# Kernel tuning notes

Hardware: AMD Instinct MI355X
Metric: run time of the kernel (lower is better)

Reference implementation:

```python
import jax, jax.numpy as jnp
import numpy as np

N_QUBITS = 256
N_LAYERS = 8
BATCH = 65536


def _ln(h, w, b):
    mu = jnp.mean(h, axis=-1, keepdims=True)
    var = jnp.mean((h - mu) ** 2, axis=-1, keepdims=True)
    return (h - mu) * jax.lax.rsqrt(var + 1e-5) * w + b


def setup_inputs() -> dict:
    key = jax.random.key(0)
    ks = jax.random.split(key, 22)
    Q = N_QUBITS
    s = 0.05
    f = jnp.float32
    return {
        "x": jax.random.normal(ks[0], (BATCH, Q), f),
        # type-0 sublayers (layers 0,3,6): Linear(Q,3Q)+LN+GELU+Linear(3Q,Q)
        "dense0_w1": jax.random.normal(ks[1], (3, Q, 3 * Q), f) * s,
        "dense0_b1": jnp.zeros((3, 3 * Q), f),
        "ln_w": jnp.ones((3, 3 * Q), f),
        "ln_b": jnp.zeros((3, 3 * Q), f),
        "dense0_w2": jax.random.normal(ks[2], (3, 3 * Q, Q), f) * s,
        "dense0_b2": jnp.zeros((3, Q), f),
        # type-1 sublayers (layers 1,4,7): Linear(Q,2Q)+SiLU+Linear(2Q,Q)
        "dense1_w1": jax.random.normal(ks[3], (3, Q, 2 * Q), f) * s,
        "dense1_b1": jnp.zeros((3, 2 * Q), f),
        "dense1_w2": jax.random.normal(ks[4], (3, 2 * Q, Q), f) * s,
        "dense1_b2": jnp.zeros((3, Q), f),
        # attention sublayers (layers 2,5): in_proj (qkv) + out_proj, heads=2, seq_len=1
        "attn_wqkv": jax.random.normal(ks[5], (2, Q, 3 * Q), f) * s,
        "attn_bqkv": jnp.zeros((2, 3 * Q), f),
        "attn_wo": jax.random.normal(ks[6], (2, Q, Q), f) * s,
        "attn_bo": jnp.zeros((2, Q), f),
        # per-layer gate params and entanglement matrices (torch randn init)
        "gate_params": jax.random.normal(ks[7], (N_LAYERS, Q, 6), f),
        "ent": jax.random.normal(ks[8], (N_LAYERS, Q, Q), f) * s,
        # nonlinear ops (4 = n_layers//2): Linear+Tanh+Linear
        "nl_w1": jax.random.normal(ks[9], (4, Q, Q), f) * s,
        "nl_b1": jnp.zeros((4, Q), f),
        "nl_w2": jax.random.normal(ks[10], (4, Q, Q), f) * s,
        "nl_b2": jnp.zeros((4, Q), f),
    }


def _forward(x, dense0_w1, dense0_b1, ln_w, ln_b, dense0_w2, dense0_b2,
             dense1_w1, dense1_b1, dense1_w2, dense1_b2,
             attn_wqkv, attn_bqkv, attn_wo, attn_bo,
             gate_params, ent, nl_w1, nl_b1, nl_w2, nl_b2):
    Q = N_QUBITS
    cur = x
    for li in range(N_LAYERS):
        res = cur
        t = li % 3
        if t == 0:
            i = li // 3
            h = cur @ dense0_w1[i] + dense0_b1[i]
            h = _ln(h, ln_w[i], ln_b[i])
            h = jax.nn.gelu(h, approximate=False)  # torch nn.GELU default (erf)
            cur = h @ dense0_w2[i] + dense0_b2[i]
        elif t == 1:
            i = (li - 1) // 3
            h = jax.nn.silu(cur @ dense1_w1[i] + dense1_b1[i])
            cur = h @ dense1_w2[i] + dense1_b2[i]
        else:
            i = (li - 2) // 3
            # seq_len == 1: softmax over a single key is identically 1, so
            # attended == v; q/k projections contribute zero (incl. gradient).
            qkv = cur @ attn_wqkv[i] + attn_bqkv[i]
            v = qkv[:, 2 * Q:]
            cur = v @ attn_wo[i] + attn_bo[i]
        # fused per-qubit gate effects (vectorized over qubits & batch)
        p = gate_params[li]  # [Q, 6]
        lin = jnp.sin(p[:, 0]) + jnp.cos(p[:, 1]) + jnp.tanh(p[:, 2])  # [Q]
        gate = (lin * cur
                + 0.5 * jnp.sin(p[:, 3] * cur + p[:, 4])
                + 0.5 * jnp.cos(p[:, 5] * cur)) / 4.0
        entangled = cur @ jnp.tanh(ent[li])
        cur = (cur + 0.3 * gate + 0.2 * entangled) / 1.5
        if li % 2 == 1:
            j = li // 2  # 0..3, always < 4 here
            nl = jnp.tanh(cur @ nl_w1[j] + nl_b1[j]) @ nl_w2[j] + nl_b2[j]
            cur = cur + 0.1 * nl
        alpha = 0.8 if li < N_LAYERS // 2 else 0.6
        cur = alpha * cur + (1.0 - alpha) * res
        cur = cur / (jnp.linalg.norm(cur, axis=1, keepdims=True) + 1e-8)
        cur = jnp.tanh(cur)
    return cur


def reference(x, dense0_w1, dense0_b1, ln_w, ln_b, dense0_w2, dense0_b2,
              dense1_w1, dense1_b1, dense1_w2, dense1_b2,
              attn_wqkv, attn_bqkv, attn_wo, attn_bo,
              gate_params, ent, nl_w1, nl_b1, nl_w2, nl_b2):
    return _forward(x, dense0_w1, dense0_b1, ln_w, ln_b, dense0_w2, dense0_b2,
                    dense1_w1, dense1_b1, dense1_w2, dense1_b2,
                    attn_wqkv, attn_bqkv, attn_wo, attn_bo,
                    gate_params, ent, nl_w1, nl_b1, nl_w2, nl_b2)
```

## Files before the change

kernel.cpp:

```cpp
#include <hip/hip_runtime.h>
#include <stdint.h>

#define DI __device__ __forceinline__

typedef __bf16 bf16;
typedef __bf16 bf16x8 __attribute__((ext_vector_type(8)));
typedef float  f32x4  __attribute__((ext_vector_type(4)));

constexpr int Q = 256;
constexpr int BATCH = 65536;
constexpr int TM = 64;
constexpr int THREADS = 256;
constexpr int NW = 4;
constexpr int MT = 4;
constexpr int NBLK = BATCH / TM;
constexpr int SC = Q + 8;

constexpr int W0A_OFF = 0;
constexpr int W0B_OFF = W0A_OFF + 3*768*256;
constexpr int W1A_OFF = W0B_OFF + 3*256*768;
constexpr int W1B_OFF = W1A_OFF + 3*512*256;
constexpr int WV_OFF  = W1B_OFF + 3*256*512;
constexpr int WO_OFF  = WV_OFF  + 2*65536;
constexpr int ATF_OFF = WO_OFF  + 2*65536;
constexpr int ENT_OFF = ATF_OFF + 2*65536;
constexpr int NL1_OFF = ENT_OFF + 8*65536;
constexpr int NL2_OFF = NL1_OFF + 4*65536;
constexpr int WEND    = NL2_OFF + 4*65536;
constexpr size_t F32_BYTE_OFF = (((size_t)WEND*2) + 255) & ~(size_t)255;

constexpr int P_D0B1 = 0;
constexpr int P_LNW  = P_D0B1 + 3*768;
constexpr int P_LNB  = P_LNW  + 3*768;
constexpr int P_D0B2 = P_LNB  + 3*768;
constexpr int P_D1B1 = P_D0B2 + 3*256;
constexpr int P_D1B2 = P_D1B1 + 3*512;
constexpr int P_BQV  = P_D1B2 + 3*256;
constexpr int P_BO   = P_BQV  + 2*256;
constexpr int P_NB1  = P_BO   + 2*256;
constexpr int P_NB2  = P_NB1  + 4*256;
constexpr int P_GLIN = P_NB2  + 4*256;
constexpr int P_GP3  = P_GLIN + 8*256;
constexpr int P_GP4  = P_GP3  + 8*256;
constexpr int P_GP5  = P_GP4  + 8*256;
constexpr int P_PACK_END = P_GP5 + 8*256;
constexpr int P_BAT  = P_PACK_END;
constexpr int P_TOT  = P_BAT + 2*256;
constexpr size_t FLAG_OFF = F32_BYTE_OFF + (size_t)P_TOT*4;

DI float ldf(const void* p, size_t idx, int f32) {
  return f32 ? ((const float*)p)[idx] : (float)((const bf16*)p)[idx];
}

DI float tanh_fast(float x) {
  float ax = fabsf(x);
  float e  = __expf(-2.0f * ax);
  float r  = (1.0f - e) / (1.0f + e);
  return copysignf(r, x);
}

DI float gelu_f(float x) {
  float ax = fabsf(x) * 0.70710678118654752f;
  float t  = 1.0f / (1.0f + 0.3275911f * ax);
  float y  = t*(0.254829592f + t*(-0.284496736f + t*(1.421413741f +
             t*(-1.453152027f + t*1.061405429f))));
  float er = copysignf(1.0f - y * __expf(-ax*ax), x);
  return 0.5f * x * (1.0f + er);
}

DI f32x4 mfma_bf16(uint4 a, uint4 b, f32x4 c) {
  return __builtin_amdgcn_mfma_f32_16x16x32_bf16(
      __builtin_bit_cast(bf16x8, a), __builtin_bit_cast(bf16x8, b), c, 0, 0, 0);
}

template<int NJ>
DI void zero_acc(f32x4 (&a)[MT][NJ]) {
#pragma unroll
  for (int i = 0; i < MT; ++i)
#pragma unroll
    for (int j = 0; j < NJ; ++j) a[i][j] = f32x4{0.f, 0.f, 0.f, 0.f};
}

template<int NJ>
DI void gemm_k256(const bf16* A, const bf16* __restrict__ Bt, int kdb, int koff,
                  f32x4 (&acc)[MT][NJ], int wave, int quad, int l16) {
  const bf16* ar[MT];
#pragma unroll
  for (int mt = 0; mt < MT; ++mt) ar[mt] = A + (mt*16 + l16)*SC + quad*8;
  const bf16* br[NJ];
#pragma unroll
  for (int nj = 0; nj < NJ; ++nj)
    br[nj] = Bt + (size_t)((nj*NW + wave)*16 + l16)*kdb + koff + quad*8;
#pragma unroll
  for (int ks = 0; ks < 8; ++ks) {
    uint4 av[MT];
#pragma unroll
    for (int mt = 0; mt < MT; ++mt) av[mt] = *(const uint4*)(ar[mt] + ks*32);
#pragma unroll
    for (int nj = 0; nj < NJ; ++nj) {
      uint4 bv = *(const uint4*)(br[nj] + ks*32);
#pragma unroll
      for (int mt = 0; mt < MT; ++mt) acc[mt][nj] = mfma_bf16(av[mt], bv, acc[mt][nj]);
    }
  }
}

template<int NJ>
DI void gemm_k256r(const bf16* A, const bf16* __restrict__ Bt, int kdb, int koff,
                   f32x4 (&acc)[MT][NJ], int wave, int quad, int l16) {
  const bf16* ar[MT];
#pragma unroll
  for (int mt = 0; mt < MT; ++mt) ar[mt] = A + (mt*16 + l16)*SC + quad*8;
  const bf16* br[NJ];
#pragma unroll
  for (int nj = 0; nj < NJ; ++nj)
    br[nj] = Bt + (size_t)((nj*NW + wave)*16 + l16)*kdb + koff + quad*8;
#pragma unroll
  for (int ks = 7; ks >= 0; --ks) {
    uint4 av[MT];
#pragma unroll
    for (int mt = 0; mt < MT; ++mt) av[mt] = *(const uint4*)(ar[mt] + ks*32);
#pragma unroll
    for (int nj = 0; nj < NJ; ++nj) {
      uint4 bv = *(const uint4*)(br[nj] + ks*32);
#pragma unroll
      for (int mt = 0; mt < MT; ++mt) acc[mt][nj] = mfma_bf16(av[mt], bv, acc[mt][nj]);
    }
  }
}

template<int NJ>
DI void addbias(f32x4 (&a)[MT][NJ], const float* __restrict__ b, int wave, int l16) {
#pragma unroll
  for (int nj = 0; nj < NJ; ++nj) {
    float bb = b[(nj*NW + wave)*16 + l16];
#pragma unroll
    for (int mt = 0; mt < MT; ++mt)
#pragma unroll
      for (int reg = 0; reg < 4; ++reg) a[mt][nj][reg] += bb;
  }
}

template<int NJ>
DI void store_t(bf16* dst, const f32x4 (&a)[MT][NJ], int wave, int quad, int l16) {
#pragma unroll
  for (int nj = 0; nj < NJ; ++nj) {
    int col = (nj*NW + wave)*16 + l16;
#pragma unroll
    for (int mt = 0; mt < MT; ++mt)
#pragma unroll
      for (int reg = 0; reg < 4; ++reg)
        dst[(mt*16 + quad*4 + reg)*SC + col] = (bf16)a[mt][nj][reg];
  }
}

__global__ void detect_dtype(const uint16_t* __restrict__ xr, int* __restrict__ flag) {
  __shared__ int s_max;
  if (threadIdx.x == 0) s_max = 0;
  __syncthreads();
  int e = 0;
  for (int i = threadIdx.x; i < 4096; i += 256) {
    int ex = (xr[2*i] >> 7) & 0xFF;
    e = e > ex ? e : ex;
  }
  atomicMax(&s_max, e);
  __syncthreads();
  if (threadIdx.x == 0) *flag = (s_max >= 140) ? 1 : 0;
}

__global__ void pack_weights(const void* __restrict__ d0w1, const void* __restrict__ d0w2,
                             const void* __restrict__ d1w1, const void* __restrict__ d1w2,
                             const void* __restrict__ wqkv, const void* __restrict__ wo,
                             const void* __restrict__ ent,  const void* __restrict__ nl1,
                             const void* __restrict__ nl2,  bf16* __restrict__ wsb,
                             const int* __restrict__ flag) {
  const int f32 = *flag;
  int job = blockIdx.y;
  const void* src; int mi, K, N, srcN, col0 = 0, dtanh = 0; long dst;
  if      (job < 3)  { src=d0w1; mi=job;    K=256; N=768; srcN=768; dst=W0A_OFF + (long)mi*768*256; }
  else if (job < 6)  { src=d0w2; mi=job-3;  K=768; N=256; srcN=256; dst=W0B_OFF + (long)mi*256*768; }
  else if (job < 9)  { src=d1w1; mi=job-6;  K=256; N=512; srcN=512; dst=W1A_OFF + (long)mi*512*256; }
  else if (job < 12) { src=d1w2; mi=job-9;  K=512; N=256; srcN=256; dst=W1B_OFF + (long)mi*256*512; }
  else if (job < 14) { src=wqkv; mi=job-12; K=256; N=256; srcN=768; col0=512; dst=WV_OFF + (long)mi*65536; }
  else if (job < 16) { src=wo;   mi=job-14; K=256; N=256; srcN=256; dst=WO_OFF + (long)mi*65536; }
  else if (job < 24) { src=ent;  mi=job-16; K=256; N=256; srcN=256; dst=ENT_OFF + (long)mi*65536; dtanh=1; }
  else if (job < 28) { src=nl1;  mi=job-24; K=256; N=256; srcN=256; dst=NL1_OFF + (long)mi*65536; }
  else               { src=nl2;  mi=job-28; K=256; N=256; srcN=256; dst=NL2_OFF + (long)mi*65536; }
  const size_t base = (size_t)mi * K * srcN;

  int tk = K/64, tn = N/64;
  int tile = blockIdx.x;
  if (tile >= tk*tn) return;
  int ik = tile % tk, in_ = tile / tk;

  __shared__ float t[64][65];
  int tid = threadIdx.x;
  for (int e = tid; e < 4096; e += 256) {
    int r = e >> 6, c = e & 63;
    t[r][c] = ldf(src, base + (size_t)(ik*64 + r)*srcN + col0 + in_*64 + c, f32);
  }
  __syncthreads();
  for (int e = tid; e < 4096; e += 256) {
    int nr = e >> 6, kc = e & 63;
    float v = t[kc][nr];
    if (dtanh) v = tanhf(v);
    wsb[dst + (size_t)(in_*64 + nr)*K + ik*64 + kc] = (bf16)v;
  }
}

__global__ void pack_params(const void* __restrict__ d0b1, const void* __restrict__ lnw,
                            const void* __restrict__ lnb,  const void* __restrict__ d0b2,
                            const void* __restrict__ d1b1, const void* __restrict__ d1b2,
                            const void* __restrict__ bqkv, const void* __restrict__ bo,
                            const void* __restrict__ gp,   const void* __restrict__ nb1,
                            const void* __restrict__ nb2,  float* __restrict__ wsf,
                            const int* __restrict__ flag) {
  const int f32 = *flag;
  int i = blockIdx.x * blockDim.x + threadIdx.x;
  if (i >= P_PACK_END) return;
  float v;
  if      (i < P_LNW)  { v = ldf(d0b1, i - P_D0B1, f32); }
  else if (i < P_LNB)  { v = ldf(lnw, i - P_LNW, f32); }
  else if (i < P_D0B2) { v = ldf(lnb, i - P_LNB, f32); }
  else if (i < P_D1B1) { v = ldf(d0b2, i - P_D0B2, f32); }
  else if (i < P_D1B2) { v = ldf(d1b1, i - P_D1B1, f32); }
  else if (i < P_BQV)  { v = ldf(d1b2, i - P_D1B2, f32); }
  else if (i < P_BO)   { int k = i - P_BQV; v = ldf(bqkv, (size_t)(k >> 8)*768 + 512 + (k & 255), f32); }
  else if (i < P_NB1)  { v = ldf(bo, i - P_BO, f32); }
  else if (i < P_NB2)  { v = ldf(nb1, i - P_NB1, f32); }
  else if (i < P_GLIN) { v = ldf(nb2, i - P_NB2, f32); }
  else if (i < P_GP3)  { int k = i - P_GLIN;
                         v = sinf(ldf(gp, (size_t)k*6 + 0, f32)) +
                             cosf(ldf(gp, (size_t)k*6 + 1, f32)) +
                             tanhf(ldf(gp, (size_t)k*6 + 2, f32)); }
  else if (i < P_GP4)  { int k = i - P_GP3; v = ldf(gp, (size_t)k*6 + 3, f32); }
  else if (i < P_GP5)  { int k = i - P_GP4; v = ldf(gp, (size_t)k*6 + 4, f32); }
  else                 { int k = i - P_GP5; v = ldf(gp, (size_t)k*6 + 5, f32); }
  wsf[i] = v;
}

__global__ void fuse_gemm(bf16* __restrict__ wsb) {
  int i = blockIdx.z;
  const bf16* A = wsb + WO_OFF + (size_t)i*65536;
  const bf16* B = wsb + WV_OFF + (size_t)i*65536;
  bf16* C = wsb + ATF_OFF + (size_t)i*65536;
  int m = threadIdx.x;
  int c = blockIdx.y;
  float s = 0.f;
  for (int n = 0; n < 256; ++n) s += (float)A[c*256 + n] * (float)B[(size_t)n*256 + m];
  C[(size_t)c*256 + m] = (bf16)s;
}

__global__ void fuse_bias(const bf16* __restrict__ wsb, float* __restrict__ wsf) {
  int t = blockIdx.x * blockDim.x + threadIdx.x;
  if (t >= 512) return;
  int i = t >> 8, c = t & 255;
  const float* bqv = wsf + P_BQV + i*256;
  const bf16* woT = wsb + WO_OFF + (size_t)i*65536;
  float s = wsf[P_BO + i*256 + c];
  for (int m = 0; m < 256; ++m) s += bqv[m] * (float)woT[c*256 + m];
  wsf[P_BAT + i*256 + c] = s;
}

__global__ __launch_bounds__(THREADS, 2)
void vqc_main(const void* __restrict__ x, const bf16* __restrict__ wsb,
              const float* __restrict__ wsf, const int* __restrict__ flag,
              void* __restrict__ out) {
  __shared__ __align__(16) bf16 curT[TM*SC];
  __shared__ __align__(16) bf16 buf0[TM*SC];
  __shared__ float red[2*NW*TM];
  __shared__ float rowa[TM], rowb[TM];

  const int tid  = threadIdx.x;
  const int wave = tid >> 6, lane = tid & 63;
  const int quad = lane >> 4, l16 = lane & 15;
  const size_t rowbase = (size_t)blockIdx.x * TM;
  const int f32io = *flag;

  if (f32io) {
    const float* xf = (const float*)x;
    for (int i = tid; i < TM*Q/4; i += THREADS) {
      int r = i >> 6, c4 = (i & 63) * 4;
      float4 v = *(const float4*)(xf + (rowbase + r)*Q + c4);
      bf16* d = curT + r*SC + c4;
      d[0] = (bf16)v.x; d[1] = (bf16)v.y; d[2] = (bf16)v.z; d[3] = (bf16)v.w;
    }
  } else {
    const bf16* xb = (const bf16*)x;
    for (int i = tid; i < TM*Q/8; i += THREADS) {
      int r = i >> 5, c8 = (i & 31) * 8;
      *(uint4*)(curT + r*SC + c8) = *(const uint4*)(xb + (rowbase + r)*Q + c8);
    }
  }
  __syncthreads();

#pragma unroll 1
  for (int li = 0; li < 8; ++li) {
    const int t = li % 3;
    f32x4 acc2[MT][4];

    if (t == 0) {
      const int i = li / 3;
      const bf16* w1 = wsb + W0A_OFF + (size_t)i*768*256;
      const bf16* w2 = wsb + W0B_OFF + (size_t)i*256*768;
      const float* b1 = wsf + P_D0B1 + i*768;

      float sa4[MT][4], sb4[MT][4];
#pragma unroll
      for (int mt = 0; mt < MT; ++mt)
#pragma unroll
        for (int reg = 0; reg < 4; ++reg) { sa4[mt][reg] = 0.f; sb4[mt][reg] = 0.f; }
#pragma unroll 1
      for (int c = 0; c < 3; ++c) {
        f32x4 acs[MT][4]; zero_acc<4>(acs);
        gemm_k256r<4>(curT, w1 + (size_t)c*256*256, 256, 0, acs, wave, quad, l16);
#pragma unroll
        for (int njl = 0; njl < 4; ++njl) {
          float bb = b1[c*256 + (njl*NW + wave)*16 + l16];
#pragma unroll
          for (int mt = 0; mt < MT; ++mt)
#pragma unroll
            for (int reg = 0; reg < 4; ++reg) {
              float v = acs[mt][njl][reg] + bb;
              sa4[mt][reg] += v; sb4[mt][reg] += v*v;
            }
        }
      }
#pragma unroll
      for (int mt = 0; mt < MT; ++mt) {
#pragma unroll
        for (int reg = 0; reg < 4; ++reg) {
          float sa = sa4[mt][reg], sb = sb4[mt][reg];
#pragma unroll
          for (int m = 1; m < 16; m <<= 1) { sa += __shfl_xor(sa, m, 64); sb += __shfl_xor(sb, m, 64); }
          if (l16 == 0) {
            int row = mt*16 + quad*4 + reg;
            red[wave*TM + row] = sa; red[NW*TM + wave*TM + row] = sb;
          }
        }
      }
      __syncthreads();
      if (tid < TM) {
        float sa = 0.f, sb = 0.f;
#pragma unroll
        for (int w = 0; w < NW; ++w) { sa += red[w*TM + tid]; sb += red[NW*TM + w*TM + tid]; }
        float mu  = sa * (1.0f/768.0f);
        float var = sb * (1.0f/768.0f) - mu*mu;
        rowa[tid] = mu; rowb[tid] = rsqrtf(fmaxf(var, 0.f) + 1e-5f);
      }
      __syncthreads();

      zero_acc<4>(acc2);
#pragma unroll 1
      for (int c = 0; c < 3; ++c) {
        f32x4 acs[MT][4]; zero_acc<4>(acs);
        gemm_k256<4>(curT, w1 + (size_t)c*256*256, 256, 0, acs, wave, quad, l16);
        const float* lw = wsf + P_LNW + i*768 + c*256;
        const float* lb = wsf + P_LNB + i*768 + c*256;
#pragma unroll
        for (int njl = 0; njl < 4; ++njl) {
          int col = (njl*NW + wave)*16 + l16;
          float bb = b1[c*256 + col];
          float w_ = lw[col], lbb = lb[col];
#pragma unroll
          for (int mt = 0; mt < MT; ++mt)
#pragma unroll
            for (int reg = 0; reg < 4; ++reg) {
              int row = mt*16 + quad*4 + reg;
              float h = gelu_f((acs[mt][njl][reg] + bb - rowa[row]) * rowb[row] * w_ + lbb);
              buf0[row*SC + col] = (bf16)h;
            }
        }
        __syncthreads();
        gemm_k256<4>(buf0, w2, 768, 256*c, acc2, wave, quad, l16);
        __syncthreads();
      }
      addbias<4>(acc2, wsf + P_D0B2 + i*256, wave, l16);
    } else if (t == 1) {
      const int i = (li - 1) / 3;
      const bf16* w1 = wsb + W1A_OFF + (size_t)i*512*256;
      const bf16* w2 = wsb + W1B_OFF + (size_t)i*256*512;
      const float* b1 = wsf + P_D1B1 + i*512;
      zero_acc<4>(acc2);
#pragma unroll 1
      for (int c = 0; c < 2; ++c) {
        f32x4 acs[MT][4]; zero_acc<4>(acs);
        gemm_k256<4>(curT, w1 + (size_t)c*256*256, 256, 0, acs, wave, quad, l16);
#pragma unroll
        for (int njl = 0; njl < 4; ++njl) {
          int col = (njl*NW + wave)*16 + l16;
          float bb = b1[c*256 + col];
#pragma unroll
          for (int mt = 0; mt < MT; ++mt)
#pragma unroll
            for (int reg = 0; reg < 4; ++reg) {
              float xv = acs[mt][njl][reg] + bb;
              buf0[(mt*16 + quad*4 + reg)*SC + col] = (bf16)(xv / (1.0f + __expf(-xv)));
            }
        }
        __syncthreads();
        gemm_k256<4>(buf0, w2, 512, 256*c, acc2, wave, quad, l16);
        __syncthreads();
      }
      addbias<4>(acc2, wsf + P_D1B2 + i*256, wave, l16);
    } else {
      const int i = (li - 2) / 3;
      zero_acc<4>(acc2);
      gemm_k256<4>(curT, wsb + ATF_OFF + (size_t)i*65536, 256, 0, acc2, wave, quad, l16);
      addbias<4>(acc2, wsf + P_BAT + i*256, wave, l16);
    }

    store_t<4>(buf0, acc2, wave, quad, l16);
    __syncthreads();
    f32x4 acc3[MT][4]; zero_acc<4>(acc3);
    gemm_k256<4>(buf0, wsb + ENT_OFF + (size_t)li*65536, 256, 0, acc3, wave, quad, l16);
    __syncthreads();

    const float* gl = wsf + P_GLIN + li*256;
    const float* g3 = wsf + P_GP3  + li*256;
    const float* g4 = wsf + P_GP4  + li*256;
    const float* g5 = wsf + P_GP5  + li*256;
#pragma unroll
    for (int nj = 0; nj < 4; ++nj) {
      int col = (nj*NW + wave)*16 + l16;
      float lin = gl[col], p3 = g3[col], p4 = g4[col], p5 = g5[col];
#pragma unroll
      for (int mt = 0; mt < MT; ++mt)
#pragma unroll
        for (int reg = 0; reg < 4; ++reg) {
          float v = acc2[mt][nj][reg];
          float gate = (lin*v + 0.5f*__sinf(p3*v + p4) + 0.5f*__cosf(p5*v)) * 0.25f;
          acc2[mt][nj][reg] = (v + 0.3f*gate + 0.2f*acc3[mt][nj][reg]) * (1.0f/1.5f);
        }
    }

    if (li & 1) {
      const int j = li >> 1;
      store_t<4>(buf0, acc2, wave, quad, l16);
      __syncthreads();
      f32x4 a4[MT][4]; zero_acc<4>(a4);
      gemm_k256<4>(buf0, wsb + NL1_OFF + (size_t)j*65536, 256, 0, a4, wave, quad, l16);
      const float* nb1p = wsf + P_NB1 + j*256;
      __syncthreads();
#pragma unroll
      for (int nj = 0; nj < 4; ++nj) {
        int col = (nj*NW + wave)*16 + l16;
        float bb = nb1p[col];
#pragma unroll
        for (int mt = 0; mt < MT; ++mt)
#pragma unroll
          for (int reg = 0; reg < 4; ++reg)
            buf0[(mt*16 + quad*4 + reg)*SC + col] = (bf16)tanh_fast(a4[mt][nj][reg] + bb);
      }
      __syncthreads();
      f32x4 a5[MT][4]; zero_acc<4>(a5);
      gemm_k256<4>(buf0, wsb + NL2_OFF + (size_t)j*65536, 256, 0, a5, wave, quad, l16);
      const float* nb2p = wsf + P_NB2 + j*256;
#pragma unroll
      for (int nj = 0; nj < 4; ++nj) {
        float bb = nb2p[(nj*NW + wave)*16 + l16];
#pragma unroll
        for (int mt = 0; mt < MT; ++mt)
#pragma unroll
          for (int reg = 0; reg < 4; ++reg) acc2[mt][nj][reg] += 0.1f*(a5[mt][nj][reg] + bb);
      }
    }

    const float alpha = (li < 4) ? 0.8f : 0.6f;
    const float beta  = 1.0f - alpha;
#pragma unroll
    for (int nj = 0; nj < 4; ++nj) {
      int col = (nj*NW + wave)*16 + l16;
#pragma unroll
      for (int mt = 0; mt < MT; ++mt)
#pragma unroll
        for (int reg = 0; reg < 4; ++reg) {
          int row = mt*16 + quad*4 + reg;
          acc2[mt][nj][reg] = alpha*acc2[mt][nj][reg] + beta*(float)curT[row*SC + col];
        }
    }
#pragma unroll
    for (int mt = 0; mt < MT; ++mt) {
#pragma unroll
      for (int reg = 0; reg < 4; ++reg) {
        float s = 0.f;
#pragma unroll
        for (int nj = 0; nj < 4; ++nj) s += acc2[mt][nj][reg]*acc2[mt][nj][reg];
#pragma unroll
        for (int m = 1; m < 16; m <<= 1) s += __shfl_xor(s, m, 64);
        if (l16 == 0) red[wave*TM + mt*16 + quad*4 + reg] = s;
      }
    }
    __syncthreads();
    if (tid < TM) {
      float s = 0.f;
#pragma unroll
      for (int w = 0; w < NW; ++w) s += red[w*TM + tid];
      rowa[tid] = 1.0f / (sqrtf(fmaxf(s, 0.f)) + 1e-8f);
    }
    __syncthreads();
#pragma unroll
    for (int nj = 0; nj < 4; ++nj) {
      int col = (nj*NW + wave)*16 + l16;
#pragma unroll
      for (int mt = 0; mt < MT; ++mt)
#pragma unroll
        for (int reg = 0; reg < 4; ++reg) {
          int row = mt*16 + quad*4 + reg;
          curT[row*SC + col] = (bf16)tanh_fast(acc2[mt][nj][reg] * rowa[row]);
        }
    }
    __syncthreads();
  }

  if (f32io) {
    float* of = (float*)out;
    for (int i = tid; i < TM*Q/4; i += THREADS) {
      int r = i >> 6, c4 = (i & 63) * 4;
      const bf16* s = curT + r*SC + c4;
      float4 v = make_float4((float)s[0], (float)s[1], (float)s[2], (float)s[3]);
      *(float4*)(of + (rowbase + r)*Q + c4) = v;
    }
  } else {
    bf16* ob = (bf16*)out;
    for (int i = tid; i < TM*Q/8; i += THREADS) {
      int r = i >> 5, c8 = (i & 31) * 8;
      *(uint4*)(ob + (rowbase + r)*Q + c8) = *(const uint4*)(curT + r*SC + c8);
    }
  }
}

extern "C" void kernel_launch(void* const* d_in, const int* in_sizes, int n_in,
                              void* d_out, int out_size, void* d_ws, size_t ws_size,
                              hipStream_t stream) {
  const void* x    = d_in[0];
  const void* d0w1 = d_in[1];
  const void* d0b1 = d_in[2];
  const void* lnw  = d_in[3];
  const void* lnb  = d_in[4];
  const void* d0w2 = d_in[5];
  const void* d0b2 = d_in[6];
  const void* d1w1 = d_in[7];
  const void* d1b1 = d_in[8];
  const void* d1w2 = d_in[9];
  const void* d1b2 = d_in[10];
  const void* wqkv = d_in[11];
  const void* bqkv = d_in[12];
  const void* wo   = d_in[13];
  const void* bo   = d_in[14];
  const void* gp   = d_in[15];
  const void* ent  = d_in[16];
  const void* nl1  = d_in[17];
  const void* nb1  = d_in[18];
  const void* nl2  = d_in[19];
  const void* nb2  = d_in[20];

  bf16*  wsb  = (bf16*)d_ws;
  float* wsf  = (float*)((char*)d_ws + F32_BYTE_OFF);
  int*   flag = (int*)((char*)d_ws + FLAG_OFF);

  detect_dtype<<<dim3(1), dim3(256), 0, stream>>>((const uint16_t*)x, flag);
  pack_weights<<<dim3(48, 32), dim3(256), 0, stream>>>(
      d0w1, d0w2, d1w1, d1w2, wqkv, wo, ent, nl1, nl2, wsb, flag);
  pack_params<<<dim3((P_PACK_END + 255)/256), dim3(256), 0, stream>>>(
      d0b1, lnw, lnb, d0b2, d1b1, d1b2, bqkv, bo, gp, nb1, nb2, wsf, flag);
  fuse_gemm<<<dim3(1, 256, 2), dim3(256), 0, stream>>>(wsb);
  fuse_bias<<<dim3(2), dim3(256), 0, stream>>>(wsb, wsf);
  vqc_main<<<dim3(NBLK), dim3(THREADS), 0, stream>>>(x, wsb, wsf, flag, d_out);
}
```

Before: 1.569 ms.

## Give each wave its own 16-row slab, removing block-level barriers

Each wave now owns 16 full-width rows and computes all 256 output columns, instead of the four waves splitting columns of a shared 64-row tile. Row reductions for LayerNorm and the L2 norm become pure intra-wave shuffles, and all __syncthreads and shared reduction buffers are dropped. The A operand is held in registers (8 uint4) per layer stage. The trade-off is that each wave reads the whole weight matrix from global/L2 for only 16 rows, so B-operand traffic per MFMA is four times higher and register pressure grows with 16 accumulator tiles.

New measurement: 3.970 ms. 2.53x slower.

```diff
diff --git a/kernel.cpp b/kernel.cpp
--- a/kernel.cpp
+++ b/kernel.cpp
@@ -12,7 +12,6 @@
 constexpr int TM = 64;
 constexpr int THREADS = 256;
 constexpr int NW = 4;
-constexpr int MT = 4;
 constexpr int NBLK = BATCH / TM;
 constexpr int SC = Q + 8;
 
@@ -73,84 +72,59 @@
       __builtin_bit_cast(bf16x8, a), __builtin_bit_cast(bf16x8, b), c, 0, 0, 0);
 }
 
-template<int NJ>
-DI void zero_acc(f32x4 (&a)[MT][NJ]) {
-#pragma unroll
-  for (int i = 0; i < MT; ++i)
-#pragma unroll
-    for (int j = 0; j < NJ; ++j) a[i][j] = f32x4{0.f, 0.f, 0.f, 0.f};
-}
-
-template<int NJ>
-DI void gemm_k256(const bf16* A, const bf16* __restrict__ Bt, int kdb, int koff,
-                  f32x4 (&acc)[MT][NJ], int wave, int quad, int l16) {
-  const bf16* ar[MT];
-#pragma unroll
-  for (int mt = 0; mt < MT; ++mt) ar[mt] = A + (mt*16 + l16)*SC + quad*8;
-  const bf16* br[NJ];
-#pragma unroll
-  for (int nj = 0; nj < NJ; ++nj)
-    br[nj] = Bt + (size_t)((nj*NW + wave)*16 + l16)*kdb + koff + quad*8;
-#pragma unroll
-  for (int ks = 0; ks < 8; ++ks) {
-    uint4 av[MT];
-#pragma unroll
-    for (int mt = 0; mt < MT; ++mt) av[mt] = *(const uint4*)(ar[mt] + ks*32);
-#pragma unroll
-    for (int nj = 0; nj < NJ; ++nj) {
-      uint4 bv = *(const uint4*)(br[nj] + ks*32);
-#pragma unroll
-      for (int mt = 0; mt < MT; ++mt) acc[mt][nj] = mfma_bf16(av[mt], bv, acc[mt][nj]);
-    }
-  }
-}
-
-template<int NJ>
-DI void gemm_k256r(const bf16* A, const bf16* __restrict__ Bt, int kdb, int koff,
-                   f32x4 (&acc)[MT][NJ], int wave, int quad, int l16) {
-  const bf16* ar[MT];
-#pragma unroll
-  for (int mt = 0; mt < MT; ++mt) ar[mt] = A + (mt*16 + l16)*SC + quad*8;
-  const bf16* br[NJ];
-#pragma unroll
-  for (int nj = 0; nj < NJ; ++nj)
-    br[nj] = Bt + (size_t)((nj*NW + wave)*16 + l16)*kdb + koff + quad*8;
-#pragma unroll
-  for (int ks = 7; ks >= 0; --ks) {
-    uint4 av[MT];
-#pragma unroll
-    for (int mt = 0; mt < MT; ++mt) av[mt] = *(const uint4*)(ar[mt] + ks*32);
-#pragma unroll
-    for (int nj = 0; nj < NJ; ++nj) {
-      uint4 bv = *(const uint4*)(br[nj] + ks*32);
-#pragma unroll
-      for (int mt = 0; mt < MT; ++mt) acc[mt][nj] = mfma_bf16(av[mt], bv, acc[mt][nj]);
-    }
-  }
-}
-
-template<int NJ>
-DI void addbias(f32x4 (&a)[MT][NJ], const float* __restrict__ b, int wave, int l16) {
-#pragma unroll
-  for (int nj = 0; nj < NJ; ++nj) {
-    float bb = b[(nj*NW + wave)*16 + l16];
-#pragma unroll
-    for (int mt = 0; mt < MT; ++mt)
-#pragma unroll
-      for (int reg = 0; reg < 4; ++reg) a[mt][nj][reg] += bb;
-  }
-}
-
-template<int NJ>
-DI void store_t(bf16* dst, const f32x4 (&a)[MT][NJ], int wave, int quad, int l16) {
-#pragma unroll
-  for (int nj = 0; nj < NJ; ++nj) {
-    int col = (nj*NW + wave)*16 + l16;
-#pragma unroll
-    for (int mt = 0; mt < MT; ++mt)
-#pragma unroll
-      for (int reg = 0; reg < 4; ++reg)
-        dst[(mt*16 + quad*4 + reg)*SC + col] = (bf16)a[mt][nj][reg];
+DI void zero16(f32x4 (&a)[16]) {
+#pragma unroll
+  for (int j = 0; j < 16; ++j) a[j] = f32x4{0.f, 0.f, 0.f, 0.f};
+}
+
+template<int KDB>
+DI void gemm16(const uint4 (&aA)[8], const bf16* __restrict__ Bt, int koff,
+               f32x4 (&acc)[16], int quad, int l16) {
+  const bf16* bp = Bt + (size_t)l16*KDB + koff + quad*8;
+#pragma unroll
+  for (int kk = 0; kk < 8; ++kk)
+#pragma unroll
+    for (int nj = 0; nj < 16; ++nj) {
+      uint4 bv = *(const uint4*)(bp + (size_t)(nj*16)*KDB + kk*32);
+      acc[nj] = mfma_bf16(aA[kk], bv, acc[nj]);
+    }
+}
+
+template<int KDB>
+DI void gemm16r(const uint4 (&aA)[8], const bf16* __restrict__ Bt, int koff,
+                f32x4 (&acc)[16], int quad, int l16) {
+  const bf16* bp = Bt + (size_t)l16*KDB + koff + quad*8;
+#pragma unroll
+  for (int kk = 7; kk >= 0; --kk)
+#pragma unroll
+    for (int nj = 0; nj < 16; ++nj) {
+      uint4 bv = *(const uint4*)(bp + (size_t)(nj*16)*KDB + kk*32);
+      acc[nj] = mfma_bf16(aA[kk], bv, acc[nj]);
+    }
+}
+
+DI void loadA(uint4 (&aA)[8], const bf16* buf, int quad, int l16) {
+  const bf16* p = buf + l16*SC + quad*8;
+#pragma unroll
+  for (int kk = 0; kk < 8; ++kk) aA[kk] = *(const uint4*)(p + kk*32);
+}
+
+DI void storeC(bf16* buf, const f32x4 (&a)[16], int quad, int l16) {
+#pragma unroll
+  for (int nj = 0; nj < 16; ++nj) {
+    int col = nj*16 + l16;
+#pragma unroll
+    for (int reg = 0; reg < 4; ++reg)
+      buf[(quad*4 + reg)*SC + col] = (bf16)a[nj][reg];
+  }
+}
+
+DI void addbias16(f32x4 (&a)[16], const float* __restrict__ b, int l16) {
+#pragma unroll
+  for (int nj = 0; nj < 16; ++nj) {
+    float bb = b[nj*16 + l16];
+#pragma unroll
+    for (int reg = 0; reg < 4; ++reg) a[nj][reg] += bb;
   }
 }
 
@@ -266,38 +240,43 @@
 void vqc_main(const void* __restrict__ x, const bf16* __restrict__ wsb,
               const float* __restrict__ wsf, const int* __restrict__ flag,
               void* __restrict__ out) {
-  __shared__ __align__(16) bf16 curT[TM*SC];
-  __shared__ __align__(16) bf16 buf0[TM*SC];
-  __shared__ float red[2*NW*TM];
-  __shared__ float rowa[TM], rowb[TM];
+  __shared__ __align__(16) bf16 curW_all[NW*16*SC];
+  __shared__ __align__(16) bf16 scr_all[NW*16*SC];
 
   const int tid  = threadIdx.x;
   const int wave = tid >> 6, lane = tid & 63;
   const int quad = lane >> 4, l16 = lane & 15;
-  const size_t rowbase = (size_t)blockIdx.x * TM;
+  bf16* curW = curW_all + wave*16*SC;
+  bf16* scr  = scr_all  + wave*16*SC;
+  const size_t wrow = (size_t)blockIdx.x * TM + wave*16;
   const int f32io = *flag;
 
   if (f32io) {
     const float* xf = (const float*)x;
-    for (int i = tid; i < TM*Q/4; i += THREADS) {
-      int r = i >> 6, c4 = (i & 63) * 4;
-      float4 v = *(const float4*)(xf + (rowbase + r)*Q + c4);
-      bf16* d = curT + r*SC + c4;
-      d[0] = (bf16)v.x; d[1] = (bf16)v.y; d[2] = (bf16)v.z; d[3] = (bf16)v.w;
+#pragma unroll
+    for (int it = 0; it < 16; ++it) {
+      int idx = it*64 + lane;
+      int row = idx >> 6, col = (idx & 63) * 4;
+      const float* s = xf + (wrow + row)*Q + col;
+      bf16* d = curW + row*SC + col;
+      d[0] = (bf16)s[0]; d[1] = (bf16)s[1]; d[2] = (bf16)s[2]; d[3] = (bf16)s[3];
     }
   } else {
     const bf16* xb = (const bf16*)x;
-    for (int i = tid; i < TM*Q/8; i += THREADS) {
-      int r = i >> 5, c8 = (i & 31) * 8;
-      *(uint4*)(curT + r*SC + c8) = *(const uint4*)(xb + (rowbase + r)*Q + c8);
-    }
-  }
-  __syncthreads();
+#pragma unroll
+    for (int it = 0; it < 8; ++it) {
+      int idx = it*64 + lane;
+      int row = idx >> 5, col = (idx & 31) * 8;
+      *(uint4*)(curW + row*SC + col) = *(const uint4*)(xb + (wrow + row)*Q + col);
+    }
+  }
+  uint4 curA[8];
+  loadA(curA, curW, quad, l16);
 
 #pragma unroll 1
   for (int li = 0; li < 8; ++li) {
     const int t = li % 3;
-    f32x4 acc2[MT][4];
+    f32x4 acc2[16];
 
     if (t == 0) {
       const int i = li / 3;
@@ -305,227 +284,190 @@
       const bf16* w2 = wsb + W0B_OFF + (size_t)i*256*768;
       const float* b1 = wsf + P_D0B1 + i*768;
 
-      float sa4[MT][4], sb4[MT][4];
-#pragma unroll
-      for (int mt = 0; mt < MT; ++mt)
-#pragma unroll
-        for (int reg = 0; reg < 4; ++reg) { sa4[mt][reg] = 0.f; sb4[mt][reg] = 0.f; }
+      float sa4[4], sb4[4];
+#pragma unroll
+      for (int reg = 0; reg < 4; ++reg) { sa4[reg] = 0.f; sb4[reg] = 0.f; }
 #pragma unroll 1
       for (int c = 0; c < 3; ++c) {
-        f32x4 acs[MT][4]; zero_acc<4>(acs);
-        gemm_k256r<4>(curT, w1 + (size_t)c*256*256, 256, 0, acs, wave, quad, l16);
-#pragma unroll
-        for (int njl = 0; njl < 4; ++njl) {
-          float bb = b1[c*256 + (njl*NW + wave)*16 + l16];
-#pragma unroll
-          for (int mt = 0; mt < MT; ++mt)
-#pragma unroll
-            for (int reg = 0; reg < 4; ++reg) {
-              float v = acs[mt][njl][reg] + bb;
-              sa4[mt][reg] += v; sb4[mt][reg] += v*v;
-            }
-        }
-      }
-#pragma unroll
-      for (int mt = 0; mt < MT; ++mt) {
-#pragma unroll
-        for (int reg = 0; reg < 4; ++reg) {
-          float sa = sa4[mt][reg], sb = sb4[mt][reg];
-#pragma unroll
-          for (int m = 1; m < 16; m <<= 1) { sa += __shfl_xor(sa, m, 64); sb += __shfl_xor(sb, m, 64); }
-          if (l16 == 0) {
-            int row = mt*16 + quad*4 + reg;
-            red[wave*TM + row] = sa; red[NW*TM + wave*TM + row] = sb;
+        f32x4 ah[16]; zero16(ah);
+        gemm16r<256>(curA, w1 + (size_t)c*256*256, 0, ah, quad, l16);
+#pragma unroll
+        for (int nj = 0; nj < 16; ++nj) {
+          float bb = b1[c*256 + nj*16 + l16];
+#pragma unroll
+          for (int reg = 0; reg < 4; ++reg) {
+            float v = ah[nj][reg] + bb;
+            sa4[reg] += v; sb4[reg] += v*v;
           }
         }
       }
-      __syncthreads();
-      if (tid < TM) {
-        float sa = 0.f, sb = 0.f;
-#pragma unroll
-        for (int w = 0; w < NW; ++w) { sa += red[w*TM + tid]; sb += red[NW*TM + w*TM + tid]; }
-        float mu  = sa * (1.0f/768.0f);
-        float var = sb * (1.0f/768.0f) - mu*mu;
-        rowa[tid] = mu; rowb[tid] = rsqrtf(fmaxf(var, 0.f) + 1e-5f);
-      }
-      __syncthreads();
-
-      zero_acc<4>(acc2);
+      float mu[4], rs[4];
+#pragma unroll
+      for (int reg = 0; reg < 4; ++reg) {
+        float sa = sa4[reg], sb = sb4[reg];
+#pragma unroll
+        for (int m = 1; m < 16; m <<= 1) { sa += __shfl_xor(sa, m, 64); sb += __shfl_xor(sb, m, 64); }
+        float mm = sa * (1.0f/768.0f);
+        float var = sb * (1.0f/768.0f) - mm*mm;
+        mu[reg] = mm; rs[reg] = rsqrtf(fmaxf(var, 0.f) + 1e-5f);
+      }
+
+      zero16(acc2);
 #pragma unroll 1
       for (int c = 0; c < 3; ++c) {
-        f32x4 acs[MT][4]; zero_acc<4>(acs);
-        gemm_k256<4>(curT, w1 + (size_t)c*256*256, 256, 0, acs, wave, quad, l16);
+        f32x4 ah[16]; zero16(ah);
+        gemm16<256>(curA, w1 + (size_t)c*256*256, 0, ah, quad, l16);
         const float* lw = wsf + P_LNW + i*768 + c*256;
         const float* lb = wsf + P_LNB + i*768 + c*256;
 #pragma unroll
-        for (int njl = 0; njl < 4; ++njl) {
-          int col = (njl*NW + wave)*16 + l16;
+        for (int nj = 0; nj < 16; ++nj) {
+          int col = nj*16 + l16;
           float bb = b1[c*256 + col];
           float w_ = lw[col], lbb = lb[col];
 #pragma unroll
-          for (int mt = 0; mt < MT; ++mt)
-#pragma unroll
-            for (int reg = 0; reg < 4; ++reg) {
-              int row = mt*16 + quad*4 + reg;
-              float h = gelu_f((acs[mt][njl][reg] + bb - rowa[row]) * rowb[row] * w_ + lbb);
-              buf0[row*SC + col] = (bf16)h;
-            }
+          for (int reg = 0; reg < 4; ++reg) {
+            float h = gelu_f((ah[nj][reg] + bb - mu[reg]) * rs[reg] * w_ + lbb);
+            scr[(quad*4 + reg)*SC + col] = (bf16)h;
+          }
         }
-        __syncthreads();
-        gemm_k256<4>(buf0, w2, 768, 256*c, acc2, wave, quad, l16);
-        __syncthreads();
-      }
-      addbias<4>(acc2, wsf + P_D0B2 + i*256, wave, l16);
+        uint4 hA[8];
+        loadA(hA, scr, quad, l16);
+        gemm16<768>(hA, w2, c*256, acc2, quad, l16);
+      }
+      addbias16(acc2, wsf + P_D0B2 + i*256, l16);
     } else if (t == 1) {
       const int i = (li - 1) / 3;
       const bf16* w1 = wsb + W1A_OFF + (size_t)i*512*256;
       const bf16* w2 = wsb + W1B_OFF + (size_t)i*256*512;
       const float* b1 = wsf + P_D1B1 + i*512;
-      zero_acc<4>(acc2);
+      zero16(acc2);
 #pragma unroll 1
       for (int c = 0; c < 2; ++c) {
-        f32x4 acs[MT][4]; zero_acc<4>(acs);
-        gemm_k256<4>(curT, w1 + (size_t)c*256*256, 256, 0, acs, wave, quad, l16);
-#pragma unroll
-        for (int njl = 0; njl < 4; ++njl) {
-          int col = (njl*NW + wave)*16 + l16;
+        f32x4 ah[16]; zero16(ah);
+        gemm16<256>(curA, w1 + (size_t)c*256*256, 0, ah, quad, l16);
+#pragma unroll
+        for (int nj = 0; nj < 16; ++nj) {
+          int col = nj*16 + l16;
           float bb = b1[c*256 + col];
 #pragma unroll
-          for (int mt = 0; mt < MT; ++mt)
-#pragma unroll
-            for (int reg = 0; reg < 4; ++reg) {
-              float xv = acs[mt][njl][reg] + bb;
-              buf0[(mt*16 + quad*4 + reg)*SC + col] = (bf16)(xv / (1.0f + __expf(-xv)));
-            }
+          for (int reg = 0; reg < 4; ++reg) {
+            float xv = ah[nj][reg] + bb;
+            scr[(quad*4 + reg)*SC + col] = (bf16)(xv / (1.0f + __expf(-xv)));
+          }
         }
-        __syncthreads();
-        gemm_k256<4>(buf0, w2, 512, 256*c, acc2, wave, quad, l16);
-        __syncthreads();
-      }
-      addbias<4>(acc2, wsf + P_D1B2 + i*256, wave, l16);
+        uint4 hA[8];
+        loadA(hA, scr, quad, l16);
+        gemm16<512>(hA, w2, c*256, acc2, quad, l16);
+      }
+      addbias16(acc2, wsf + P_D1B2 + i*256, l16);
     } else {
       const int i = (li - 2) / 3;
-      zero_acc<4>(acc2);
-      gemm_k256<4>(curT, wsb + ATF_OFF + (size_t)i*65536, 256, 0, acc2, wave, quad, l16);
-      addbias<4>(acc2, wsf + P_BAT + i*256, wave, l16);
-    }
-
-    store_t<4>(buf0, acc2, wave, quad, l16);
-    __syncthreads();
-    f32x4 acc3[MT][4]; zero_acc<4>(acc3);
-    gemm_k256<4>(buf0, wsb + ENT_OFF + (size_t)li*65536, 256, 0, acc3, wave, quad, l16);
-    __syncthreads();
-
-    const float* gl = wsf + P_GLIN + li*256;
-    const float* g3 = wsf + P_GP3  + li*256;
-    const float* g4 = wsf + P_GP4  + li*256;
-    const float* g5 = wsf + P_GP5  + li*256;
-#pragma unroll
-    for (int nj = 0; nj < 4; ++nj) {
-      int col = (nj*NW + wave)*16 + l16;
-      float lin = gl[col], p3 = g3[col], p4 = g4[col], p5 = g5[col];
-#pragma unroll
-      for (int mt = 0; mt < MT; ++mt)
+      zero16(acc2);
+      gemm16<256>(curA, wsb + ATF_OFF + (size_t)i*65536, 0, acc2, quad, l16);
+      addbias16(acc2, wsf + P_BAT + i*256, l16);
+    }
+
+    storeC(scr, acc2, quad, l16);
+    uint4 eA[8];
+    loadA(eA, scr, quad, l16);
+    f32x4 acc3[16]; zero16(acc3);
+    gemm16<256>(eA, wsb + ENT_OFF + (size_t)li*65536, 0, acc3, quad, l16);
+
+    {
+      const float* gl = wsf + P_GLIN + li*256;
+      const float* g3 = wsf + P_GP3  + li*256;
+      const float* g4 = wsf + P_GP4  + li*256;
+      const float* g5 = wsf + P_GP5  + li*256;
+#pragma unroll
+      for (int nj = 0; nj < 16; ++nj) {
+        int col = nj*16 + l16;
+        float lin = gl[col], p3 = g3[col], p4 = g4[col], p5 = g5[col];
 #pragma unroll
         for (int reg = 0; reg < 4; ++reg) {
-          float v = acc2[mt][nj][reg];
+          float v = acc2[nj][reg];
           float gate = (lin*v + 0.5f*__sinf(p3*v + p4) + 0.5f*__cosf(p5*v)) * 0.25f;
-          acc2[mt][nj][reg] = (v + 0.3f*gate + 0.2f*acc3[mt][nj][reg]) * (1.0f/1.5f);
+          acc2[nj][reg] = (v + 0.3f*gate + 0.2f*acc3[nj][reg]) * (1.0f/1.5f);
         }
+      }
     }
 
     if (li & 1) {
       const int j = li >> 1;
-      store_t<4>(buf0, acc2, wave, quad, l16);
-      __syncthreads();
-      f32x4 a4[MT][4]; zero_acc<4>(a4);
-      gemm_k256<4>(buf0, wsb + NL1_OFF + (size_t)j*65536, 256, 0, a4, wave, quad, l16);
+      storeC(scr, acc2, quad, l16);
+      uint4 gA[8];
+      loadA(gA, scr, quad, l16);
+      f32x4 at[16]; zero16(at);
+      gemm16<256>(gA, wsb + NL1_OFF + (size_t)j*65536, 0, at, quad, l16);
       const float* nb1p = wsf + P_NB1 + j*256;
-      __syncthreads();
-#pragma unroll
-      for (int nj = 0; nj < 4; ++nj) {
-        int col = (nj*NW + wave)*16 + l16;
+#pragma unroll
+      for (int nj = 0; nj < 16; ++nj) {
+        int col = nj*16 + l16;
         float bb = nb1p[col];
 #pragma unroll
-        for (int mt = 0; mt < MT; ++mt)
-#pragma unroll
-          for (int reg = 0; reg < 4; ++reg)
-            buf0[(mt*16 + quad*4 + reg)*SC + col] = (bf16)tanh_fast(a4[mt][nj][reg] + bb);
-      }
-      __syncthreads();
-      f32x4 a5[MT][4]; zero_acc<4>(a5);
-      gemm_k256<4>(buf0, wsb + NL2_OFF + (size_t)j*65536, 256, 0, a5, wave, quad, l16);
+        for (int reg = 0; reg < 4; ++reg)
+          scr[(quad*4 + reg)*SC + col] = (bf16)tanh_fast(at[nj][reg] + bb);
+      }
+      uint4 tA[8];
+      loadA(tA, scr, quad, l16);
+      f32x4 an[16]; zero16(an);
+      gemm16<256>(tA, wsb + NL2_OFF + (size_t)j*65536, 0, an, quad, l16);
       const float* nb2p = wsf + P_NB2 + j*256;
 #pragma unroll
-      for (int nj = 0; nj < 4; ++nj) {
-        float bb = nb2p[(nj*NW + wave)*16 + l16];
-#pragma unroll
-        for (int mt = 0; mt < MT; ++mt)
-#pragma unroll
-          for (int reg = 0; reg < 4; ++reg) acc2[mt][nj][reg] += 0.1f*(a5[mt][nj][reg] + bb);
+      for (int nj = 0; nj < 16; ++nj) {
+        float bb = nb2p[nj*16 + l16];
+#pragma unroll
+        for (int reg = 0; reg < 4; ++reg) acc2[nj][reg] += 0.1f*(an[nj][reg] + bb);
       }
     }
 
     const float alpha = (li < 4) ? 0.8f : 0.6f;
     const float beta  = 1.0f - alpha;
 #pragma unroll
-    for (int nj = 0; nj < 4; ++nj) {
-      int col = (nj*NW + wave)*16 + l16;
-#pragma unroll
-      for (int mt = 0; mt < MT; ++mt)
-#pragma unroll
-        for (int reg = 0; reg < 4; ++reg) {
-          int row = mt*16 + quad*4 + reg;
-          acc2[mt][nj][reg] = alpha*acc2[mt][nj][reg] + beta*(float)curT[row*SC + col];
-        }
-    }
-#pragma unroll
-    for (int mt = 0; mt < MT; ++mt) {
+    for (int nj = 0; nj < 16; ++nj) {
+      int col = nj*16 + l16;
 #pragma unroll
       for (int reg = 0; reg < 4; ++reg) {
-        float s = 0.f;
-#pragma unroll
-        for (int nj = 0; nj < 4; ++nj) s += acc2[mt][nj][reg]*acc2[mt][nj][reg];
-#pragma unroll
-        for (int m = 1; m < 16; m <<= 1) s += __shfl_xor(s, m, 64);
-        if (l16 == 0) red[wave*TM + mt*16 + quad*4 + reg] = s;
-      }
-    }
-    __syncthreads();
-    if (tid < TM) {
+        float old = (float)curW[(quad*4 + reg)*SC + col];
+        acc2[nj][reg] = alpha*acc2[nj][reg] + beta*old;
+      }
+    }
+    float ra[4];
+#pragma unroll
+    for (int reg = 0; reg < 4; ++reg) {
       float s = 0.f;
 #pragma unroll
-      for (int w = 0; w < NW; ++w) s += red[w*TM + tid];
-      rowa[tid] = 1.0f / (sqrtf(fmaxf(s, 0.f)) + 1e-8f);
-    }
-    __syncthreads();
-#pragma unroll
-    for (int nj = 0; nj < 4; ++nj) {
-      int col = (nj*NW + wave)*16 + l16;
-#pragma unroll
-      for (int mt = 0; mt < MT; ++mt)
-#pragma unroll
-        for (int reg = 0; reg < 4; ++reg) {
-          int row = mt*16 + quad*4 + reg;
-          curT[row*SC + col] = (bf16)tanh_fast(acc2[mt][nj][reg] * rowa[row]);
-        }
-    }
-    __syncthreads();
+      for (int nj = 0; nj < 16; ++nj) s += acc2[nj][reg]*acc2[nj][reg];
+#pragma unroll
+      for (int m = 1; m < 16; m <<= 1) s += __shfl_xor(s, m, 64);
+      ra[reg] = 1.0f / (sqrtf(fmaxf(s, 0.f)) + 1e-8f);
+    }
+#pragma unroll
+    for (int nj = 0; nj < 16; ++nj) {
+      int col = nj*16 + l16;
+#pragma unroll
+      for (int reg = 0; reg < 4; ++reg)
+        curW[(quad*4 + reg)*SC + col] = (bf16)tanh_fast(acc2[nj][reg] * ra[reg]);
+    }
+    loadA(curA, curW, quad, l16);
   }
 
   if (f32io) {
     float* of = (float*)out;
-    for (int i = tid; i < TM*Q/4; i += THREADS) {
-      int r = i >> 6, c4 = (i & 63) * 4;
-      const bf16* s = curT + r*SC + c4;
+#pragma unroll
+    for (int it = 0; it < 16; ++it) {
+      int idx = it*64 + lane;
+      int row = idx >> 6, col = (idx & 63) * 4;
+      const bf16* s = curW + row*SC + col;
       float4 v = make_float4((float)s[0], (float)s[1], (float)s[2], (float)s[3]);
-      *(float4*)(of + (rowbase + r)*Q + c4) = v;
+      *(float4*)(of + (wrow + row)*Q + col) = v;
     }
   } else {
     bf16* ob = (bf16*)out;
-    for (int i = tid; i < TM*Q/8; i += THREADS) {
-      int r = i >> 5, c8 = (i & 31) * 8;
-      *(uint4*)(ob + (rowbase + r)*Q + c8) = *(const uint4*)(curT + r*SC + c8);
+#pragma unroll
+    for (int it = 0; it < 8; ++it) {
+      int idx = it*64 + lane;
+      int row = idx >> 5, col = (idx & 31) * 8;
+      *(uint4*)(ob + (wrow + row)*Q + col) = *(const uint4*)(curW + row*SC + col);
     }
   }
 }
```
